# Kernel optimization log

Measured on AMD Instinct MI355X. Metric: run time of the kernel, lower is better.

The kernel has to match this reference:

```python
import jax, jax.numpy as jnp
import numpy as np

N, E, B = 3000, 96000, 64
CIN, MID = 8, 16
G1, G2 = 32, 8
FC1, FC2, OUT = 512, 128, 10
EPS = 1e-5


def setup_inputs() -> dict:
    key = jax.random.key(0)
    ks = jax.random.split(key, 40)
    u = lambda k, shape, s: jax.random.uniform(k, shape, jnp.float32, -s, s)
    inp = {}
    inp['x'] = jax.random.normal(ks[0], (N, B, CIN), jnp.float32)
    inp['edge_index'] = jax.random.randint(ks[1], (2, E), 0, N, jnp.int64)
    # SAGEConv params (uniform(-1/sqrt(in_channels), ...))
    s = 1.0 / np.sqrt(CIN)
    inp['edge_w_raw'] = jnp.ones((E,), jnp.float32) * 0.01
    inp['sage_self_w'] = u(ks[2], (CIN, MID), s)
    inp['sage_w'] = u(ks[3], (CIN, MID), s)
    inp['sage_b'] = u(ks[4], (MID,), s)
    # LayerNorm over (num_nodes, mid_channel)
    inp['ln_g'] = jnp.ones((N, MID), jnp.float32)
    inp['ln_b'] = jnp.zeros((N, MID), jnp.float32)
    # 1x1 Conv2d stacks (stored as [out,in] matrices) + BatchNorm2d (eval stats)
    inp['conv1_w'] = jax.random.normal(ks[5], (G1, MID), jnp.float32) * np.sqrt(2.0 / G1)
    inp['conv1_b'] = u(ks[6], (G1,), 1.0 / np.sqrt(MID))
    inp['bn1_g'] = jax.random.uniform(ks[7], (G1,), jnp.float32, 0.5, 1.5)
    inp['bn1_b'] = jax.random.normal(ks[8], (G1,), jnp.float32) * 0.1
    inp['bn1_m'] = jax.random.normal(ks[9], (G1,), jnp.float32) * 0.1
    inp['bn1_v'] = jax.random.uniform(ks[10], (G1,), jnp.float32, 0.5, 1.5)
    inp['conv2_w'] = jax.random.normal(ks[11], (G2, G1), jnp.float32) * np.sqrt(2.0 / G2)
    inp['conv2_b'] = u(ks[12], (G2,), 1.0 / np.sqrt(G1))
    inp['bn2_g'] = jax.random.uniform(ks[13], (G2,), jnp.float32, 0.5, 1.5)
    inp['bn2_b'] = jax.random.normal(ks[14], (G2,), jnp.float32) * 0.1
    inp['bn2_m'] = jax.random.normal(ks[15], (G2,), jnp.float32) * 0.1
    inp['bn2_v'] = jax.random.uniform(ks[16], (G2,), jnp.float32, 0.5, 1.5)
    # FC stack: Linear(G2*N, FC1) + BN1d, Linear(FC1, FC2) + BN1d, fc1
    d0 = G2 * N
    inp['fc_w1'] = jax.random.normal(ks[17], (FC1, d0), jnp.float32) * np.sqrt(2.0 / (d0 + FC1))
    inp['fc_b1'] = jnp.full((FC1,), 0.01, jnp.float32)
    inp['bnf1_g'] = jax.random.uniform(ks[18], (FC1,), jnp.float32, 0.5, 1.5)
    inp['bnf1_b'] = jax.random.normal(ks[19], (FC1,), jnp.float32) * 0.1
    inp['bnf1_m'] = jax.random.normal(ks[20], (FC1,), jnp.float32) * 0.1
    inp['bnf1_v'] = jax.random.uniform(ks[21], (FC1,), jnp.float32, 0.5, 1.5)
    inp['fc_w2'] = jax.random.normal(ks[22], (FC2, FC1), jnp.float32) * np.sqrt(2.0 / (FC1 + FC2))
    inp['fc_b2'] = jnp.full((FC2,), 0.01, jnp.float32)
    inp['bnf2_g'] = jax.random.uniform(ks[23], (FC2,), jnp.float32, 0.5, 1.5)
    inp['bnf2_b'] = jax.random.normal(ks[24], (FC2,), jnp.float32) * 0.1
    inp['bnf2_m'] = jax.random.normal(ks[25], (FC2,), jnp.float32) * 0.1
    inp['bnf2_v'] = jax.random.uniform(ks[26], (FC2,), jnp.float32, 0.5, 1.5)
    inp['fc1_w'] = jax.random.normal(ks[27], (OUT, FC2), jnp.float32) * np.sqrt(2.0 / (FC2 + OUT))
    inp['fc1_b'] = jnp.full((OUT,), 0.01, jnp.float32)
    return inp


def _bn(y, g, b, m, v):
    # eval-mode BatchNorm; y is [B, C, N] or [B, C]
    if y.ndim == 3:
        return (y - m[:, None]) * (g[:, None] / jnp.sqrt(v[:, None] + EPS)) + b[:, None]
    return (y - m) * (g / jnp.sqrt(v + EPS)) + b


def reference(x, edge_index, edge_w_raw, sage_self_w, sage_w, sage_b, ln_g, ln_b,
              conv1_w, conv1_b, bn1_g, bn1_b, bn1_m, bn1_v,
              conv2_w, conv2_b, bn2_g, bn2_b, bn2_m, bn2_v,
              fc_w1, fc_b1, bnf1_g, bnf1_b, bnf1_m, bnf1_v,
              fc_w2, fc_b2, bnf2_g, bnf2_b, bnf2_m, bnf2_v,
              fc1_w, fc1_b):
    row, col = edge_index[0], edge_index[1]
    ew = jax.nn.sigmoid(edge_w_raw)
    # SAGEConv: gather -> weighted message -> scatter-mean by col -> matmul
    msg = x[row] * ew[:, None, None]                          # [E, B, CIN]
    summed = jax.ops.segment_sum(msg, col, num_segments=N)    # [N, B, CIN]
    cnt = jax.ops.segment_sum(jnp.ones((E,), x.dtype), col, num_segments=N)
    agg = summed / jnp.maximum(cnt, 1.0)[:, None, None]
    neigh = jnp.einsum('nbc,cm->nbm', agg, sage_w) + sage_b   # [N, B, MID]
    self_out = jnp.einsum('nbc,cm->nbm', x, sage_self_w)
    h = 0.0 * self_out + 1.0 * neigh                          # alphas = [0, 1]
    h = jax.nn.relu(h)
    # LayerNorm over (num_nodes, mid) per batch element
    hb = jnp.transpose(h, (1, 0, 2))                          # [B, N, MID]
    mu = hb.mean(axis=(1, 2), keepdims=True)
    var = hb.var(axis=(1, 2), keepdims=True)
    hb = (hb - mu) / jnp.sqrt(var + EPS) * ln_g + ln_b
    y = jnp.transpose(hb, (0, 2, 1))                          # [B, MID, N]
    # 1x1 conv stack (relu then BN, matching source order)
    y = jnp.einsum('om,bmn->bon', conv1_w, y) + conv1_b[:, None]
    y = _bn(jax.nn.relu(y), bn1_g, bn1_b, bn1_m, bn1_v)
    y = jnp.einsum('oc,bcn->bon', conv2_w, y) + conv2_b[:, None]
    y = _bn(jax.nn.relu(y), bn2_g, bn2_b, bn2_m, bn2_v)       # [B, G2, N]
    z = y.reshape(y.shape[0], -1)                             # [B, G2*N]
    z = jax.nn.relu(_bn(z @ fc_w1.T + fc_b1, bnf1_g, bnf1_b, bnf1_m, bnf1_v))
    z = jax.nn.relu(_bn(z @ fc_w2.T + fc_b2, bnf2_g, bnf2_b, bnf2_m, bnf2_v))
    logits = z @ fc1_w.T + fc1_b
    return jax.nn.softmax(logits, axis=-1), logits
```

## Files before the change

### kernel.cpp

```cpp
#include <hip/hip_runtime.h>
#include <hip/hip_bf16.h>
#include <math.h>

#define NN   3000
#define EE   96000
#define BB   64
#define CIN  8
#define MID  16
#define G1   32
#define G2   8
#define FC1N 512
#define FC2N 128
#define OUTN 10
#define EPSV 1e-5f

#define BC   (BB * CIN)
#define HROW (NN * MID)
#define D0   (G2 * NN)

#define P_EWRAW 0
#define P_SW    96000
#define P_SB    96128
#define P_LNG   96144
#define P_LNB   144144
#define P_C1W   192144
#define P_C1B   192656
#define P_BN1G  192688
#define P_BN1B  192720
#define P_BN1M  192752
#define P_BN1V  192784
#define P_C2W   192816
#define P_C2B   193072
#define P_BN2G  193080
#define P_BN2B  193088
#define P_BN2M  193096
#define P_BN2V  193104
#define P_FB1   193112
#define P_BF1G  193624
#define P_BF1B  194136
#define P_BF1M  194648
#define P_BF1V  195160
#define P_FW2   195672
#define P_FB2   261208
#define P_BF2G  261336
#define P_BF2B  261464
#define P_BF2M  261592
#define P_BF2V  261720
#define P_FOW   261848
#define P_FOB   263128
#define P_TOT   263138

#define KCH  320
#define NKC  75

__device__ __forceinline__ float b2f(unsigned short u) {
    union { unsigned int i; float f; } c;
    c.i = ((unsigned int)u) << 16;
    return c.f;
}

__device__ __forceinline__ unsigned short f2b_rne(float x) {
    union { float f; unsigned int u; } c; c.f = x;
    unsigned int r = c.u + 0x7FFFu + ((c.u >> 16) & 1u);
    return (unsigned short)(r >> 16);
}

typedef __attribute__((ext_vector_type(8))) short short8;
typedef __attribute__((ext_vector_type(4))) float f32x4;

struct PTab { const void* p[30]; };
__global__ __launch_bounds__(256)
void k_prep(const void* __restrict__ ei_raw, const unsigned int* __restrict__ ewr,
            const void* __restrict__ xr, PTab tab,
            int* __restrict__ ei32, int* __restrict__ cnt, int* __restrict__ flags,
            float* __restrict__ x32, float* __restrict__ P) {
    __shared__ int sh_is64, sh_bf;
    if (threadIdx.x == 0) {
        const int* pw = (const int*)ei_raw;
        int any = 0;
        #pragma unroll
        for (int i = 1; i < 32; i += 2) any |= pw[i];
        sh_is64 = (any == 0) ? 1 : 0;
        unsigned int w = ewr[0];
        sh_bf = ((w >> 16) == (w & 0xFFFFu)) ? 1 : 0;
        if (blockIdx.x == 0) flags[0] = sh_bf;
    }
    __syncthreads();
    int bf = sh_bf;
    long long gi = (long long)blockIdx.x * blockDim.x + threadIdx.x;
    if (gi < 2 * EE) {
        int i = (int)gi;
        int v = sh_is64 ? (int)((const long long*)ei_raw)[i]
                        : ((const int*)ei_raw)[i];
        ei32[i] = v;
        if (i >= EE) atomicAdd(&cnt[v], 1);
        return;
    }
    gi -= 2 * EE;
    if (gi < NN * BC) {
        int i = (int)gi;
        x32[i] = bf ? b2f(((const unsigned short*)xr)[i]) : ((const float*)xr)[i];
        return;
    }
    gi -= NN * BC;
    if (gi >= P_TOT) return;
    int i = (int)gi;
    const int off[31] = {
        P_EWRAW, P_SW, P_SB, P_LNG, P_LNB, P_C1W, P_C1B, P_BN1G, P_BN1B, P_BN1M,
        P_BN1V, P_C2W, P_C2B, P_BN2G, P_BN2B, P_BN2M, P_BN2V, P_FB1, P_BF1G,
        P_BF1B, P_BF1M, P_BF1V, P_FW2, P_FB2, P_BF2G, P_BF2B, P_BF2M, P_BF2V,
        P_FOW, P_FOB, P_TOT };
    int r = 0;
    #pragma unroll
    for (int j = 1; j < 31; ++j) r += (i >= off[j]) ? 1 : 0;
    int e = i - off[r];
    P[i] = bf ? b2f(((const unsigned short*)tab.p[r])[e])
              : ((const float*)tab.p[r])[e];
}

__global__ void k_scan(const int* __restrict__ cnt, int* __restrict__ off,
                       int* __restrict__ cursor) {
    __shared__ int part[1024];
    int t = threadIdx.x;
    int base = t * 3;
    int c0 = 0, c1 = 0, c2 = 0;
    if (base     < NN) c0 = cnt[base];
    if (base + 1 < NN) c1 = cnt[base + 1];
    if (base + 2 < NN) c2 = cnt[base + 2];
    int s = c0 + c1 + c2;
    part[t] = s;
    __syncthreads();
    for (int d = 1; d < 1024; d <<= 1) {
        int v = (t >= d) ? part[t - d] : 0;
        __syncthreads();
        part[t] += v;
        __syncthreads();
    }
    int excl = part[t] - s;
    if (base < NN)     { off[base]     = excl;           cursor[base]     = excl; }
    if (base + 1 < NN) { off[base + 1] = excl + c0;      cursor[base + 1] = excl + c0; }
    if (base + 2 < NN) { off[base + 2] = excl + c0 + c1; cursor[base + 2] = excl + c0 + c1; }
    if (t == 1023) off[NN] = part[1023];
}

__global__ void k_scatter(const int* __restrict__ ei, const float* __restrict__ ew,
                          int* __restrict__ cursor,
                          int* __restrict__ rcsr, float* __restrict__ wcsr) {
    int e = blockIdx.x * blockDim.x + threadIdx.x;
    if (e < EE) {
        int p = atomicAdd(&cursor[ei[EE + e]], 1);
        rcsr[p] = ei[e];
        wcsr[p] = 1.f / (1.f + expf(-ew[e]));
    }
}

__global__ __launch_bounds__(256)
void k_agg_sage(const float* __restrict__ x,
                const int* __restrict__ off,
                const int* __restrict__ rcsr, const float* __restrict__ wcsr,
                const float* __restrict__ sw, const float* __restrict__ sb,
                float* __restrict__ hb) {
    __shared__ float aggL[BC];
    __shared__ float swL[CIN * MID];
    __shared__ float sbL[MID];
    int n = blockIdx.x;
    int t = threadIdx.x;
    if (t < CIN * MID) swL[t] = sw[t];
    if (t < MID)       sbL[t] = sb[t];
    int k0 = off[n], k1 = off[n + 1];
    float a0 = 0.f, a1 = 0.f, b0 = 0.f, b1 = 0.f;
    int k = k0;
    for (; k + 3 < k1; k += 4) {
        int   r0 = rcsr[k],     r1 = rcsr[k + 1];
        int   r2 = rcsr[k + 2], r3 = rcsr[k + 3];
        float w0 = wcsr[k],     w1 = wcsr[k + 1];
        float w2 = wcsr[k + 2], w3 = wcsr[k + 3];
        const float* xp0 = x + (size_t)r0 * BC;
        const float* xp1 = x + (size_t)r1 * BC;
        const float* xp2 = x + (size_t)r2 * BC;
        const float* xp3 = x + (size_t)r3 * BC;
        a0 += xp0[t]       * w0;  a1 += xp0[t + 256] * w0;
        b0 += xp1[t]       * w1;  b1 += xp1[t + 256] * w1;
        a0 += xp2[t]       * w2;  a1 += xp2[t + 256] * w2;
        b0 += xp3[t]       * w3;  b1 += xp3[t + 256] * w3;
    }
    for (; k < k1; ++k) {
        int r0 = rcsr[k];
        float w0 = wcsr[k];
        const float* xp0 = x + (size_t)r0 * BC;
        a0 += xp0[t] * w0;
        a1 += xp0[t + 256] * w0;
    }
    float inv = 1.f / fmaxf((float)(k1 - k0), 1.f);
    aggL[t]       = (a0 + b0) * inv;
    aggL[t + 256] = (a1 + b1) * inv;
    __syncthreads();
    #pragma unroll
    for (int r4 = 0; r4 < 4; ++r4) {
        int q = t + r4 * 256;
        int b = q >> 4, m = q & 15;
        float v = sbL[m];
        const float* ag = &aggL[b * CIN];
        #pragma unroll
        for (int c = 0; c < CIN; ++c) v += ag[c] * swL[c * MID + m];
        v = fmaxf(v, 0.f);
        hb[(size_t)b * HROW + n * MID + m] = v;
    }
}

__global__ __launch_bounds__(256)
void k_ln_stats(const float* __restrict__ hb, float* __restrict__ stats) {
    __shared__ float ssum[256], ssq[256];
    int b = blockIdx.x, t = threadIdx.x;
    const float4* p = (const float4*)(hb + (size_t)b * HROW);
    float s = 0.f, q = 0.f;
    for (int i = t; i < HROW / 4; i += 256) {
        float4 v = p[i];
        s += v.x + v.y + v.z + v.w;
        q += v.x * v.x + v.y * v.y + v.z * v.z + v.w * v.w;
    }
    ssum[t] = s; ssq[t] = q;
    __syncthreads();
    for (int d = 128; d > 0; d >>= 1) {
        if (t < d) { ssum[t] += ssum[t + d]; ssq[t] += ssq[t + d]; }
        __syncthreads();
    }
    if (t == 0) {
        float mu = ssum[0] / (float)HROW;
        float var = ssq[0] / (float)HROW - mu * mu;
        stats[b]      = mu;
        stats[BB + b] = 1.f / sqrtf(var + EPSV);
    }
}

__global__ __launch_bounds__(256)
void k_conv_stack(const float* __restrict__ hb, const float* __restrict__ stats,
                  const float* __restrict__ P, float* __restrict__ zT) {
    __shared__ float hbt[64 * 65];
    __shared__ float w1s[G1 * MID], w2s[G2 * G1];
    __shared__ float c1s[G1], s1[G1], t1[G1];
    __shared__ float c2s[G2], s2[G2], t2[G2];
    int t = threadIdx.x;
    int n0 = blockIdx.x * 4;
    for (int j = t; j < G1 * MID; j += 256) w1s[j] = P[P_C1W + j];
    if (t < G2 * G1)  w2s[t] = P[P_C2W + t];
    if (t < G1) {
        float s = P[P_BN1G + t] / sqrtf(P[P_BN1V + t] + EPSV);
        c1s[t] = P[P_C1B + t]; s1[t] = s; t1[t] = P[P_BN1B + t] - P[P_BN1M + t] * s;
    }
    if (t < G2) {
        float s = P[P_BN2G + t] / sqrtf(P[P_BN2V + t] + EPSV);
        c2s[t] = P[P_C2B + t]; s2[t] = s; t2[t] = P[P_BN2B + t] - P[P_BN2M + t] * s;
    }
    #pragma unroll
    for (int r = 0; r < 4; ++r) {
        int i = r * 256 + t;
        int b = i >> 4, q = i & 15;
        float4 v = *(const float4*)(hb + (size_t)b * HROW + n0 * MID + q * 4);
        int ld = b * 65 + q * 4;
        hbt[ld] = v.x; hbt[ld + 1] = v.y; hbt[ld + 2] = v.z; hbt[ld + 3] = v.w;
    }
    __syncthreads();
    int nl = t >> 6, b = t & 63;
    int n = n0 + nl;
    float mu = stats[b], rs = stats[BB + b];
    float tv[MID];
    #pragma unroll
    for (int m = 0; m < MID; ++m) {
        float g = P[P_LNG + n * MID + m], lb = P[P_LNB + n * MID + m];
        tv[m] = (hbt[b * 65 + nl * MID + m] - mu) * rs * g + lb;
    }
    float v1[G1];
    #pragma unroll
    for (int o = 0; o < G1; ++o) {
        float d = c1s[o];
        #pragma unroll
        for (int m = 0; m < MID; ++m) d += w1s[o * MID + m] * tv[m];
        d = fmaxf(d, 0.f);
        v1[o] = d * s1[o] + t1[o];
    }
    #pragma unroll
    for (int o2 = 0; o2 < G2; ++o2) {
        float d = c2s[o2];
        #pragma unroll
        for (int c = 0; c < G1; ++c) d += w2s[o2 * G1 + c] * v1[c];
        d = fmaxf(d, 0.f);
        zT[((size_t)(o2 * NN + n)) * BB + b] = d * s2[o2] + t2[o2];
    }
}

__global__ __launch_bounds__(256)
void k_fc1(const float* __restrict__ zT, const void* __restrict__ w1raw,
           const int* __restrict__ flags, float* __restrict__ out1p) {
    __shared__ unsigned int zs[64 * 20];
    int kc = blockIdx.y;
    int t = threadIdx.x;
    int lane = t & 63;
    int wv = t >> 6;
    int n = lane & 15;
    int q = lane >> 4;
    int fbase = blockIdx.x * 64 + wv * 16;
    int bf = flags[0];
    const size_t kcb = (size_t)kc * KCH;
    const float*          w1f = (const float*)w1raw;
    const unsigned short* w1b = (const unsigned short*)w1raw;

    f32x4 acc0 = {0.f, 0.f, 0.f, 0.f};
    f32x4 acc1 = {0.f, 0.f, 0.f, 0.f};
    f32x4 acc2 = {0.f, 0.f, 0.f, 0.f};
    f32x4 acc3 = {0.f, 0.f, 0.f, 0.f};

    int zb = t & 63;
    int kg = t >> 6;

    for (int ks = 0; ks < KCH / 32; ++ks) {
        size_t k0 = kcb + (size_t)ks * 32;
        const float* zsrc = zT + k0 * BB + zb;
        float zv[8];
        #pragma unroll
        for (int j = 0; j < 8; ++j) zv[j] = zsrc[(kg * 8 + j) * BB];
        unsigned int pk0 = (unsigned int)f2b_rne(zv[0]) | ((unsigned int)f2b_rne(zv[1]) << 16);
        unsigned int pk1 = (unsigned int)f2b_rne(zv[2]) | ((unsigned int)f2b_rne(zv[3]) << 16);
        unsigned int pk2 = (unsigned int)f2b_rne(zv[4]) | ((unsigned int)f2b_rne(zv[5]) << 16);
        unsigned int pk3 = (unsigned int)f2b_rne(zv[6]) | ((unsigned int)f2b_rne(zv[7]) << 16);
        __syncthreads();
        *(uint4*)&zs[zb * 20 + kg * 4] = make_uint4(pk0, pk1, pk2, pk3);
        short8 av;
        if (bf) {
            av = *(const short8*)(w1b + (size_t)(fbase + n) * D0 + k0 + q * 8);
        } else {
            const float* wr = w1f + (size_t)(fbase + n) * D0 + k0 + q * 8;
            float4 wa = *(const float4*)wr;
            float4 wb = *(const float4*)(wr + 4);
            av[0] = (short)f2b_rne(wa.x); av[1] = (short)f2b_rne(wa.y);
            av[2] = (short)f2b_rne(wa.z); av[3] = (short)f2b_rne(wa.w);
            av[4] = (short)f2b_rne(wb.x); av[5] = (short)f2b_rne(wb.y);
            av[6] = (short)f2b_rne(wb.z); av[7] = (short)f2b_rne(wb.w);
        }
        __syncthreads();
        const char* zbase = (const char*)zs + q * 16;
        short8 bv0 = *(const short8*)(zbase + (0  + n) * 80);
        short8 bv1 = *(const short8*)(zbase + (16 + n) * 80);
        short8 bv2 = *(const short8*)(zbase + (32 + n) * 80);
        short8 bv3 = *(const short8*)(zbase + (48 + n) * 80);
        acc0 = __builtin_amdgcn_mfma_f32_16x16x32_bf16(av, bv0, acc0, 0, 0, 0);
        acc1 = __builtin_amdgcn_mfma_f32_16x16x32_bf16(av, bv1, acc1, 0, 0, 0);
        acc2 = __builtin_amdgcn_mfma_f32_16x16x32_bf16(av, bv2, acc2, 0, 0, 0);
        acc3 = __builtin_amdgcn_mfma_f32_16x16x32_bf16(av, bv3, acc3, 0, 0, 0);
    }
    float* op = out1p + ((size_t)kc * FC1N + fbase + q * 4) * BB + n;
    #pragma unroll
    for (int r = 0; r < 4; ++r) {
        op[r * BB +  0] = acc0[r];
        op[r * BB + 16] = acc1[r];
        op[r * BB + 32] = acc2[r];
        op[r * BB + 48] = acc3[r];
    }
}

__global__ void k_fc1_fin(const float* __restrict__ out1p, const float* __restrict__ P,
                          float* __restrict__ z1) {
    int i = blockIdx.x * blockDim.x + threadIdx.x;
    if (i < BB * FC1N) {
        int f = i >> 6, b = i & 63;
        float acc = 0.f;
        for (int kc = 0; kc < NKC; ++kc)
            acc += out1p[((size_t)kc * FC1N + f) * BB + b];
        acc += P[P_FB1 + f];
        float s = P[P_BF1G + f] / sqrtf(P[P_BF1V + f] + EPSV);
        acc = (acc - P[P_BF1M + f]) * s + P[P_BF1B + f];
        z1[b * FC1N + f] = fmaxf(acc, 0.f);
    }
}

__global__ __launch_bounds__(128)
void k_fc2head(const float* __restrict__ z1, const float* __restrict__ P,
               const int* __restrict__ flags, void* __restrict__ outv) {
    __shared__ float zsrc[FC1N];
    __shared__ float z2s[FC2N];
    __shared__ float lg[OUTN];
    __shared__ float red[2];
    int b = blockIdx.x, t = threadIdx.x;
    #pragma unroll
    for (int r = 0; r < 4; ++r) zsrc[t + r * 128] = z1[b * FC1N + t + r * 128];
    __syncthreads();
    {
        int f = t;
        const float4* wr = (const float4*)(P + P_FW2 + (size_t)f * FC1N);
        const float4* zr = (const float4*)zsrc;
        float acc = P[P_FB2 + f];
        for (int k = 0; k < FC1N / 4; ++k) {
            float4 wv = wr[k];
            float4 zv = zr[k];
            acc += wv.x * zv.x + wv.y * zv.y + wv.z * zv.z + wv.w * zv.w;
        }
        float s = P[P_BF2G + f] / sqrtf(P[P_BF2V + f] + EPSV);
        acc = (acc - P[P_BF2M + f]) * s + P[P_BF2B + f];
        z2s[f] = fmaxf(acc, 0.f);
    }
    __syncthreads();
    if (t < OUTN) {
        float acc = P[P_FOB + t];
        const float* wr = P + P_FOW + t * FC2N;
        for (int k = 0; k < FC2N; ++k) acc += wr[k] * z2s[k];
        lg[t] = acc;
    }
    __syncthreads();
    if (t == 0) {
        float mx = lg[0];
        for (int o = 1; o < OUTN; ++o) mx = fmaxf(mx, lg[o]);
        float s = 0.f;
        for (int o = 0; o < OUTN; ++o) s += expf(lg[o] - mx);
        red[0] = mx; red[1] = s;
    }
    __syncthreads();
    if (t < OUTN) {
        float p = expf(lg[t] - red[0]) / red[1];
        if (flags[0]) {
            __hip_bfloat16* o = (__hip_bfloat16*)outv;
            o[b * OUTN + t] = __float2bfloat16(p);
            o[BB * OUTN + b * OUTN + t] = __float2bfloat16(lg[t]);
        } else {
            float* o = (float*)outv;
            o[b * OUTN + t] = p;
            o[BB * OUTN + b * OUTN + t] = lg[t];
        }
    }
}

extern "C" void kernel_launch(void* const* d_in, const int* in_sizes, int n_in,
                              void* d_out, int out_size, void* d_ws, size_t ws_size,
                              hipStream_t stream) {
    char* ws = (char*)d_ws;
    size_t o = 0;
    auto carve = [&](size_t bytes) { void* p = ws + o; o += (bytes + 255) & ~(size_t)255; return p; };
    int*   flags  = (int*)  carve(16);
    int*   ei32   = (int*)  carve((size_t)2 * EE * sizeof(int));
    int*   cnt    = (int*)  carve(NN * sizeof(int));
    int*   off    = (int*)  carve((NN + 1) * sizeof(int));
    int*   cursor = (int*)  carve(NN * sizeof(int));
    int*   rcsr   = (int*)  carve(EE * sizeof(int));
    float* wcsr   = (float*)carve(EE * sizeof(float));
    float* P      = (float*)carve((size_t)P_TOT * sizeof(float));
    float* x32    = (float*)carve((size_t)NN * BC * sizeof(float));
    float* hb     = (float*)carve((size_t)BB * HROW * sizeof(float));
    float* stats  = (float*)carve(2 * BB * sizeof(float));
    float* zT     = (float*)carve((size_t)D0 * BB * sizeof(float));
    float* out1p  = (float*)carve((size_t)NKC * FC1N * BB * sizeof(float));
    float* z1     = (float*)carve(BB * FC1N * sizeof(float));

    hipMemsetAsync(cnt, 0, NN * sizeof(int), stream);

    PTab tab;
    tab.p[0]  = d_in[2];   tab.p[1]  = d_in[4];   tab.p[2]  = d_in[5];
    tab.p[3]  = d_in[6];   tab.p[4]  = d_in[7];   tab.p[5]  = d_in[8];
    tab.p[6]  = d_in[9];   tab.p[7]  = d_in[10];  tab.p[8]  = d_in[11];
    tab.p[9]  = d_in[12];  tab.p[10] = d_in[13];  tab.p[11] = d_in[14];
    tab.p[12] = d_in[15];  tab.p[13] = d_in[16];  tab.p[14] = d_in[17];
    tab.p[15] = d_in[18];  tab.p[16] = d_in[19];  tab.p[17] = d_in[21];
    tab.p[18] = d_in[22];  tab.p[19] = d_in[23];  tab.p[20] = d_in[24];
    tab.p[21] = d_in[25];  tab.p[22] = d_in[26];  tab.p[23] = d_in[27];
    tab.p[24] = d_in[28];  tab.p[25] = d_in[29];  tab.p[26] = d_in[30];
    tab.p[27] = d_in[31];  tab.p[28] = d_in[32];  tab.p[29] = d_in[33];

    long long prep_tot = 2LL * EE + (long long)NN * BC + P_TOT;
    k_prep<<<(int)((prep_tot + 255) / 256), 256, 0, stream>>>(
        d_in[1], (const unsigned int*)d_in[2], d_in[0], tab,
        ei32, cnt, flags, x32, P);

    k_scan   <<<1, 1024, 0, stream>>>(cnt, off, cursor);
    k_scatter<<<(EE + 255) / 256, 256, 0, stream>>>(ei32, P + P_EWRAW, cursor, rcsr, wcsr);
    k_agg_sage<<<NN, 256, 0, stream>>>(x32, off, rcsr, wcsr, P + P_SW, P + P_SB, hb);
    k_ln_stats<<<BB, 256, 0, stream>>>(hb, stats);
    k_conv_stack<<<NN / 4, 256, 0, stream>>>(hb, stats, P, zT);
    dim3 g7(FC1N / 64, NKC);
    k_fc1    <<<g7, 256, 0, stream>>>(zT, d_in[20], flags, out1p);
    k_fc1_fin<<<(BB * FC1N + 255) / 256, 256, 0, stream>>>(out1p, P, z1);
    k_fc2head<<<BB, 128, 0, stream>>>(z1, P, flags, (void*)d_out);
}
```

Measured before the change: 266.0 us.

## Read raw x directly in aggregation and store conv output as bf16

Drops the fp32 copy of x made in the prep kernel and has the aggregation kernel gather straight from the raw input, decoding bf16 pairs in-register when the input is bf16. It also makes the conv stack write its output already rounded to bf16, so the FC1 kernel reads half the bytes and skips the per-element conversion. This cuts a full pass over x and halves zT traffic, at the cost of a runtime branch in the aggregation kernel and earlier rounding of the activations.

```diff
diff --git a/kernel.cpp b/kernel.cpp
--- a/kernel.cpp
+++ b/kernel.cpp
@@ -71,9 +71,9 @@
 struct PTab { const void* p[30]; };
 __global__ __launch_bounds__(256)
 void k_prep(const void* __restrict__ ei_raw, const unsigned int* __restrict__ ewr,
-            const void* __restrict__ xr, PTab tab,
+            PTab tab,
             int* __restrict__ ei32, int* __restrict__ cnt, int* __restrict__ flags,
-            float* __restrict__ x32, float* __restrict__ P) {
+            float* __restrict__ P) {
     __shared__ int sh_is64, sh_bf;
     if (threadIdx.x == 0) {
         const int* pw = (const int*)ei_raw;
@@ -97,12 +97,6 @@
         return;
     }
     gi -= 2 * EE;
-    if (gi < NN * BC) {
-        int i = (int)gi;
-        x32[i] = bf ? b2f(((const unsigned short*)xr)[i]) : ((const float*)xr)[i];
-        return;
-    }
-    gi -= NN * BC;
     if (gi >= P_TOT) return;
     int i = (int)gi;
     const int off[31] = {
@@ -155,7 +149,7 @@
 }
 
 __global__ __launch_bounds__(256)
-void k_agg_sage(const float* __restrict__ x,
+void k_agg_sage(const void* __restrict__ xraw, const int* __restrict__ flags,
                 const int* __restrict__ off,
                 const int* __restrict__ rcsr, const float* __restrict__ wcsr,
                 const float* __restrict__ sw, const float* __restrict__ sb,
@@ -170,30 +164,63 @@
     int k0 = off[n], k1 = off[n + 1];
     float a0 = 0.f, a1 = 0.f, b0 = 0.f, b1 = 0.f;
     int k = k0;
-    for (; k + 3 < k1; k += 4) {
-        int   r0 = rcsr[k],     r1 = rcsr[k + 1];
-        int   r2 = rcsr[k + 2], r3 = rcsr[k + 3];
-        float w0 = wcsr[k],     w1 = wcsr[k + 1];
-        float w2 = wcsr[k + 2], w3 = wcsr[k + 3];
-        const float* xp0 = x + (size_t)r0 * BC;
-        const float* xp1 = x + (size_t)r1 * BC;
-        const float* xp2 = x + (size_t)r2 * BC;
-        const float* xp3 = x + (size_t)r3 * BC;
-        a0 += xp0[t]       * w0;  a1 += xp0[t + 256] * w0;
-        b0 += xp1[t]       * w1;  b1 += xp1[t + 256] * w1;
-        a0 += xp2[t]       * w2;  a1 += xp2[t + 256] * w2;
-        b0 += xp3[t]       * w3;  b1 += xp3[t + 256] * w3;
-    }
-    for (; k < k1; ++k) {
-        int r0 = rcsr[k];
-        float w0 = wcsr[k];
-        const float* xp0 = x + (size_t)r0 * BC;
-        a0 += xp0[t] * w0;
-        a1 += xp0[t + 256] * w0;
-    }
-    float inv = 1.f / fmaxf((float)(k1 - k0), 1.f);
-    aggL[t]       = (a0 + b0) * inv;
-    aggL[t + 256] = (a1 + b1) * inv;
+    if (flags[0]) {
+        const unsigned int* xu = (const unsigned int*)xraw;
+        for (; k + 3 < k1; k += 4) {
+            int   r0 = rcsr[k],     r1 = rcsr[k + 1];
+            int   r2 = rcsr[k + 2], r3 = rcsr[k + 3];
+            float w0 = wcsr[k],     w1 = wcsr[k + 1];
+            float w2 = wcsr[k + 2], w3 = wcsr[k + 3];
+            unsigned int u0 = xu[(size_t)r0 * 256 + t];
+            unsigned int u1 = xu[(size_t)r1 * 256 + t];
+            unsigned int u2 = xu[(size_t)r2 * 256 + t];
+            unsigned int u3 = xu[(size_t)r3 * 256 + t];
+            a0 += b2f((unsigned short)(u0 & 0xFFFFu)) * w0;
+            a1 += b2f((unsigned short)(u0 >> 16))     * w0;
+            b0 += b2f((unsigned short)(u1 & 0xFFFFu)) * w1;
+            b1 += b2f((unsigned short)(u1 >> 16))     * w1;
+            a0 += b2f((unsigned short)(u2 & 0xFFFFu)) * w2;
+            a1 += b2f((unsigned short)(u2 >> 16))     * w2;
+            b0 += b2f((unsigned short)(u3 & 0xFFFFu)) * w3;
+            b1 += b2f((unsigned short)(u3 >> 16))     * w3;
+        }
+        for (; k < k1; ++k) {
+            int r0 = rcsr[k];
+            float w0 = wcsr[k];
+            unsigned int u0 = xu[(size_t)r0 * 256 + t];
+            a0 += b2f((unsigned short)(u0 & 0xFFFFu)) * w0;
+            a1 += b2f((unsigned short)(u0 >> 16))     * w0;
+        }
+        float inv = 1.f / fmaxf((float)(k1 - k0), 1.f);
+        aggL[2 * t]     = (a0 + b0) * inv;
+        aggL[2 * t + 1] = (a1 + b1) * inv;
+    } else {
+        const float* x = (const float*)xraw;
+        for (; k + 3 < k1; k += 4) {
+            int   r0 = rcsr[k],     r1 = rcsr[k + 1];
+            int   r2 = rcsr[k + 2], r3 = rcsr[k + 3];
+            float w0 = wcsr[k],     w1 = wcsr[k + 1];
+            float w2 = wcsr[k + 2], w3 = wcsr[k + 3];
+            const float* xp0 = x + (size_t)r0 * BC;
+            const float* xp1 = x + (size_t)r1 * BC;
+            const float* xp2 = x + (size_t)r2 * BC;
+            const float* xp3 = x + (size_t)r3 * BC;
+            a0 += xp0[t]       * w0;  a1 += xp0[t + 256] * w0;
+            b0 += xp1[t]       * w1;  b1 += xp1[t + 256] * w1;
+            a0 += xp2[t]       * w2;  a1 += xp2[t + 256] * w2;
+            b0 += xp3[t]       * w3;  b1 += xp3[t + 256] * w3;
+        }
+        for (; k < k1; ++k) {
+            int r0 = rcsr[k];
+            float w0 = wcsr[k];
+            const float* xp0 = x + (size_t)r0 * BC;
+            a0 += xp0[t] * w0;
+            a1 += xp0[t + 256] * w0;
+        }
+        float inv = 1.f / fmaxf((float)(k1 - k0), 1.f);
+        aggL[t]       = (a0 + b0) * inv;
+        aggL[t + 256] = (a1 + b1) * inv;
+    }
     __syncthreads();
     #pragma unroll
     for (int r4 = 0; r4 < 4; ++r4) {
@@ -235,7 +262,7 @@
 
 __global__ __launch_bounds__(256)
 void k_conv_stack(const float* __restrict__ hb, const float* __restrict__ stats,
-                  const float* __restrict__ P, float* __restrict__ zT) {
+                  const float* __restrict__ P, unsigned short* __restrict__ zT) {
     __shared__ float hbt[64 * 65];
     __shared__ float w1s[G1 * MID], w2s[G2 * G1];
     __shared__ float c1s[G1], s1[G1], t1[G1];
@@ -285,12 +312,12 @@
         #pragma unroll
         for (int c = 0; c < G1; ++c) d += w2s[o2 * G1 + c] * v1[c];
         d = fmaxf(d, 0.f);
-        zT[((size_t)(o2 * NN + n)) * BB + b] = d * s2[o2] + t2[o2];
+        zT[((size_t)(o2 * NN + n)) * BB + b] = f2b_rne(d * s2[o2] + t2[o2]);
     }
 }
 
 __global__ __launch_bounds__(256)
-void k_fc1(const float* __restrict__ zT, const void* __restrict__ w1raw,
+void k_fc1(const unsigned short* __restrict__ zT, const void* __restrict__ w1raw,
            const int* __restrict__ flags, float* __restrict__ out1p) {
     __shared__ unsigned int zs[64 * 20];
     int kc = blockIdx.y;
@@ -315,14 +342,14 @@
 
     for (int ks = 0; ks < KCH / 32; ++ks) {
         size_t k0 = kcb + (size_t)ks * 32;
-        const float* zsrc = zT + k0 * BB + zb;
-        float zv[8];
+        const unsigned short* zsrc = zT + (k0 + kg * 8) * BB + zb;
+        unsigned short zv[8];
         #pragma unroll
-        for (int j = 0; j < 8; ++j) zv[j] = zsrc[(kg * 8 + j) * BB];
-        unsigned int pk0 = (unsigned int)f2b_rne(zv[0]) | ((unsigned int)f2b_rne(zv[1]) << 16);
-        unsigned int pk1 = (unsigned int)f2b_rne(zv[2]) | ((unsigned int)f2b_rne(zv[3]) << 16);
-        unsigned int pk2 = (unsigned int)f2b_rne(zv[4]) | ((unsigned int)f2b_rne(zv[5]) << 16);
-        unsigned int pk3 = (unsigned int)f2b_rne(zv[6]) | ((unsigned int)f2b_rne(zv[7]) << 16);
+        for (int j = 0; j < 8; ++j) zv[j] = zsrc[j * BB];
+        unsigned int pk0 = (unsigned int)zv[0] | ((unsigned int)zv[1] << 16);
+        unsigned int pk1 = (unsigned int)zv[2] | ((unsigned int)zv[3] << 16);
+        unsigned int pk2 = (unsigned int)zv[4] | ((unsigned int)zv[5] << 16);
+        unsigned int pk3 = (unsigned int)zv[6] | ((unsigned int)zv[7] << 16);
         __syncthreads();
         *(uint4*)&zs[zb * 20 + kg * 4] = make_uint4(pk0, pk1, pk2, pk3);
         short8 av;
@@ -442,10 +469,9 @@
     int*   rcsr   = (int*)  carve(EE * sizeof(int));
     float* wcsr   = (float*)carve(EE * sizeof(float));
     float* P      = (float*)carve((size_t)P_TOT * sizeof(float));
-    float* x32    = (float*)carve((size_t)NN * BC * sizeof(float));
     float* hb     = (float*)carve((size_t)BB * HROW * sizeof(float));
     float* stats  = (float*)carve(2 * BB * sizeof(float));
-    float* zT     = (float*)carve((size_t)D0 * BB * sizeof(float));
+    unsigned short* zT = (unsigned short*)carve((size_t)D0 * BB * sizeof(unsigned short));
     float* out1p  = (float*)carve((size_t)NKC * FC1N * BB * sizeof(float));
     float* z1     = (float*)carve(BB * FC1N * sizeof(float));
 
@@ -463,14 +489,14 @@
     tab.p[24] = d_in[28];  tab.p[25] = d_in[29];  tab.p[26] = d_in[30];
     tab.p[27] = d_in[31];  tab.p[28] = d_in[32];  tab.p[29] = d_in[33];
 
-    long long prep_tot = 2LL * EE + (long long)NN * BC + P_TOT;
+    long long prep_tot = 2LL * EE + P_TOT;
     k_prep<<<(int)((prep_tot + 255) / 256), 256, 0, stream>>>(
-        d_in[1], (const unsigned int*)d_in[2], d_in[0], tab,
-        ei32, cnt, flags, x32, P);
+        d_in[1], (const unsigned int*)d_in[2], tab, ei32, cnt, flags, P);
 
     k_scan   <<<1, 1024, 0, stream>>>(cnt, off, cursor);
     k_scatter<<<(EE + 255) / 256, 256, 0, stream>>>(ei32, P + P_EWRAW, cursor, rcsr, wcsr);
-    k_agg_sage<<<NN, 256, 0, stream>>>(x32, off, rcsr, wcsr, P + P_SW, P + P_SB, hb);
+    k_agg_sage<<<NN, 256, 0, stream>>>(d_in[0], flags, off, rcsr, wcsr,
+                                       P + P_SW, P + P_SB, hb);
     k_ln_stats<<<BB, 256, 0, stream>>>(hb, stats);
     k_conv_stack<<<NN / 4, 256, 0, stream>>>(hb, stats, P, zT);
     dim3 g7(FC1N / 64, NKC);
```

Result: faster. 259.8 us (-2.3%).
